# Kernel tuning notes

Hardware: AMD Instinct MI355X
Metric: run time of the kernel (lower is better)

The kernel has to match this reference:

```python
import jax, jax.numpy as jnp
import numpy as np

B, N, D, H = 8, 1024, 768, 12
HD = D // H


def setup_inputs() -> dict:
    key = jax.random.key(0)
    ks = jax.random.split(key, 13)
    s = 0.02
    return {
        "q": jax.random.normal(ks[0], (B, N, D), jnp.float32),
        "k": jax.random.normal(ks[1], (B, N, D), jnp.float32),
        "v": jax.random.normal(ks[2], (B, N, D), jnp.float32),
        "attn_bias": jax.random.normal(ks[3], (B, H, N, N), jnp.float32),
        "attn_mask": jnp.ones((B, N, N), jnp.int32),
        "Wq": jax.random.normal(ks[4], (D, D), jnp.float32) * s,
        "bq": jnp.zeros((D,), jnp.float32),
        "Wk": jax.random.normal(ks[5], (D, D), jnp.float32) * s,
        "bk": jnp.zeros((D,), jnp.float32),
        "Wv": jax.random.normal(ks[6], (D, D), jnp.float32) * s,
        "bv": jnp.zeros((D,), jnp.float32),
        "Wo": jax.random.normal(ks[7], (D, D), jnp.float32) * s,
        "bo": jnp.zeros((D,), jnp.float32),
    }


def reference(q, k, v, attn_bias, attn_mask, Wq, bq, Wk, bk, Wv, bv, Wo, bo):
    scale = jnp.sqrt(jnp.float32(HD))
    # projections; nn.Linear computes x @ W.T + b
    qh = (q @ Wq.T + bq).reshape(B, N, H, HD).transpose(0, 2, 1, 3)  # [B,H,N,hd]
    kh = (k @ Wk.T + bk).reshape(B, N, H, HD).transpose(0, 2, 1, 3)
    vh = (v @ Wv.T + bv).reshape(B, N, H, HD).transpose(0, 2, 1, 3)
    attn = jnp.einsum("bhqd,bhkd->bhqk", qh, kh) / scale
    attn = attn + attn_bias  # Graphormer edge/spatial bias
    attn = jnp.where(attn_mask[:, None, :, :] == 0, -jnp.inf, attn)
    attn = jax.nn.softmax(attn, axis=-1)
    out = jnp.einsum("bhqk,bhkd->bhqd", attn, vh)  # [B,H,N,hd]
    out = out.transpose(0, 2, 1, 3).reshape(B, N, D)
    return out @ Wo.T + bo
```

## Files before the change

### kernel.cpp

```cpp
#include <hip/hip_runtime.h>
#include <hip/hip_bf16.h>

using f32x4  = __attribute__((ext_vector_type(4))) float;
using i32x4  = __attribute__((ext_vector_type(4))) int;
using bf16x8 = __attribute__((ext_vector_type(8))) short;
using bf16x4 = __attribute__((ext_vector_type(4))) short;

constexpr int BATCH = 8, SEQ = 1024, DIM = 768, NHEAD = 12, HDIM = 64;
constexpr int MROWS = BATCH * SEQ;

__device__ __forceinline__ short f2bf(float f) {
    union { float f; unsigned u; } x; x.f = f;
    unsigned r = (x.u + 0x7fffu + ((x.u >> 16) & 1u)) >> 16;
    return (short)r;
}
__device__ __forceinline__ float fexp2(float x) { return __builtin_amdgcn_exp2f(x); }

__device__ __forceinline__ bf16x8 cvt8(const float* p) {
    const f32x4 x0 = *(const f32x4*)p;
    const f32x4 x1 = *(const f32x4*)(p + 4);
    bf16x8 r;
    #pragma unroll
    for (int j = 0; j < 4; ++j) { r[j] = f2bf(x0[j]); r[4 + j] = f2bf(x1[j]); }
    return r;
}

__device__ __forceinline__ long kfrag_addr(int tok, int dd) {
    return ((long)(tok >> 6)) * 4096 + ((tok & 63) >> 4) * 1024 + (dd >> 5) * 512
         + ((dd >> 3) & 3) * 128 + (tok & 15) * 8 + (dd & 7);
}
__device__ __forceinline__ long vfrag_addr(int tok, int dd) {
    return ((long)(tok >> 6)) * 4096 + (dd >> 4) * 1024 + ((tok >> 5) & 1) * 512
         + ((tok >> 3) & 3) * 128 + (dd & 15) * 8 + (tok & 7);
}

__global__ __launch_bounds__(256)
void cvt3(const float* __restrict__ a, const float* __restrict__ b,
          const float* __restrict__ c, short* __restrict__ oa,
          short* __restrict__ ob, short* __restrict__ oc, int n8) {
    const int stride = gridDim.x * 256;
    for (int i = blockIdx.x * 256 + threadIdx.x; i < n8; i += stride) {
        const long base = (long)i * 8;
        *(bf16x8*)(oa + base) = cvt8(a + base);
        *(bf16x8*)(ob + base) = cvt8(b + base);
        *(bf16x8*)(oc + base) = cvt8(c + base);
    }
}

__global__ __launch_bounds__(256)
void cvt4(const float* __restrict__ a, const float* __restrict__ b,
          const float* __restrict__ c, const float* __restrict__ d,
          short* __restrict__ oa, short* __restrict__ ob,
          short* __restrict__ oc, short* __restrict__ od, int n8) {
    const int stride = gridDim.x * 256;
    for (int i = blockIdx.x * 256 + threadIdx.x; i < n8; i += stride) {
        const long base = (long)i * 8;
        *(bf16x8*)(oa + base) = cvt8(a + base);
        *(bf16x8*)(ob + base) = cvt8(b + base);
        *(bf16x8*)(oc + base) = cvt8(c + base);
        *(bf16x8*)(od + base) = cvt8(d + base);
    }
}

__global__ __launch_bounds__(256, 4)
void gemm_qkv(const short* __restrict__ qb, const short* __restrict__ kb,
              const short* __restrict__ vbp,
              const short* __restrict__ Wqb, const short* __restrict__ Wkb,
              const short* __restrict__ Wvb,
              const float* __restrict__ bq, const float* __restrict__ bk,
              const float* __restrict__ bv,
              short* __restrict__ Qp, short* __restrict__ Kp, short* __restrict__ Vp) {
    constexpr int K  = DIM;
    constexpr int NT = DIM / 128;
    __shared__ short As[128][72];
    __shared__ short Bs[128][72];

    const int sub = blockIdx.x % 3;
    const int bid = blockIdx.x / 3;
    const short* A = sub == 0 ? qb : sub == 1 ? kb : vbp;
    const short* W = sub == 0 ? Wqb : sub == 1 ? Wkb : Wvb;
    const float* bias = sub == 0 ? bq : sub == 1 ? bk : bv;

    const int bm = bid / NT, bn = bid % NT;
    const int m0 = bm * 128, n0 = bn * 128;
    const int t = threadIdx.x;
    const int lane = t & 63, w = t >> 6;
    const int wm = (w >> 1) * 64, wn = (w & 1) * 64;
    const int l16 = lane & 15, lg = lane >> 4;

    const int sr = t >> 1, sc = (t & 1) * 16;
    const short* aptr = A + (long)(m0 + sr) * K + sc;
    const short* wptr = W + (long)(n0 + sr) * K + sc;

    bf16x8 ra0 = *(const bf16x8*)(aptr);
    bf16x8 ra1 = *(const bf16x8*)(aptr + 8);
    bf16x8 rw0 = *(const bf16x8*)(wptr);
    bf16x8 rw1 = *(const bf16x8*)(wptr + 8);

    f32x4 acc[4][4] = {};

    for (int k0 = 0; k0 < K; k0 += 32) {
        *(bf16x8*)&As[sr][sc]     = ra0;
        *(bf16x8*)&As[sr][sc + 8] = ra1;
        *(bf16x8*)&Bs[sr][sc]     = rw0;
        *(bf16x8*)&Bs[sr][sc + 8] = rw1;
        if (k0 + 32 < K) {
            ra0 = *(const bf16x8*)(aptr + k0 + 32);
            ra1 = *(const bf16x8*)(aptr + k0 + 40);
            rw0 = *(const bf16x8*)(wptr + k0 + 32);
            rw1 = *(const bf16x8*)(wptr + k0 + 40);
        }
        __syncthreads();

        bf16x8 af[4], bfg[4];
        const int kc = lg * 8;
        #pragma unroll
        for (int mi = 0; mi < 4; ++mi)
            af[mi] = *(const bf16x8*)&As[wm + mi * 16 + l16][kc];
        #pragma unroll
        for (int ni = 0; ni < 4; ++ni)
            bfg[ni] = *(const bf16x8*)&Bs[wn + ni * 16 + l16][kc];
        #pragma unroll
        for (int mi = 0; mi < 4; ++mi)
            #pragma unroll
            for (int ni = 0; ni < 4; ++ni)
                acc[mi][ni] = __builtin_amdgcn_mfma_f32_16x16x32_bf16(
                    af[mi], bfg[ni], acc[mi][ni], 0, 0, 0);
        __syncthreads();
    }

    #pragma unroll
    for (int mi = 0; mi < 4; ++mi) {
        const int row = m0 + wm + mi * 16 + lg * 4;
        const int bb = row / SEQ;
        #pragma unroll
        for (int ni = 0; ni < 4; ++ni) {
            const int col = n0 + wn + ni * 16 + l16;
            const float bv = bias[col];
            const int hh = col >> 6, dd = col & 63;
            #pragma unroll
            for (int j = 0; j < 4; ++j) {
                float val = acc[mi][ni][j] + bv;
                if (sub == 0) {
                    Qp[(long)(row + j) * DIM + col] = f2bf(val * 0.125f);
                } else {
                    const int tok = (row % SEQ) + j;
                    const long pbase = (long)(bb * NHEAD + hh) * 65536;
                    if (sub == 1)
                        Kp[pbase + kfrag_addr(tok, dd)] = f2bf(val);
                    else
                        Vp[pbase + vfrag_addr(tok, dd)] = f2bf(val);
                }
            }
        }
    }
}

__global__ __launch_bounds__(256, 4)
void gemm_out(const short* __restrict__ A, const short* __restrict__ W,
              const float* __restrict__ bias, float* __restrict__ Cout) {
    constexpr int K  = DIM;
    constexpr int NT = DIM / 128;
    __shared__ short As[128][72];
    __shared__ short Bs[128][72];

    const int bm = blockIdx.x / NT, bn = blockIdx.x % NT;
    const int m0 = bm * 128, n0 = bn * 128;
    const int t = threadIdx.x;
    const int lane = t & 63, w = t >> 6;
    const int wm = (w >> 1) * 64, wn = (w & 1) * 64;
    const int l16 = lane & 15, lg = lane >> 4;

    const int sr = t >> 1, sc = (t & 1) * 16;
    const short* aptr = A + (long)(m0 + sr) * K + sc;
    const short* wptr = W + (long)(n0 + sr) * K + sc;

    bf16x8 ra0 = *(const bf16x8*)(aptr);
    bf16x8 ra1 = *(const bf16x8*)(aptr + 8);
    bf16x8 rw0 = *(const bf16x8*)(wptr);
    bf16x8 rw1 = *(const bf16x8*)(wptr + 8);

    f32x4 acc[4][4] = {};

    for (int k0 = 0; k0 < K; k0 += 32) {
        *(bf16x8*)&As[sr][sc]     = ra0;
        *(bf16x8*)&As[sr][sc + 8] = ra1;
        *(bf16x8*)&Bs[sr][sc]     = rw0;
        *(bf16x8*)&Bs[sr][sc + 8] = rw1;
        if (k0 + 32 < K) {
            ra0 = *(const bf16x8*)(aptr + k0 + 32);
            ra1 = *(const bf16x8*)(aptr + k0 + 40);
            rw0 = *(const bf16x8*)(wptr + k0 + 32);
            rw1 = *(const bf16x8*)(wptr + k0 + 40);
        }
        __syncthreads();

        bf16x8 af[4], bfg[4];
        const int kc = lg * 8;
        #pragma unroll
        for (int mi = 0; mi < 4; ++mi)
            af[mi] = *(const bf16x8*)&As[wm + mi * 16 + l16][kc];
        #pragma unroll
        for (int ni = 0; ni < 4; ++ni)
            bfg[ni] = *(const bf16x8*)&Bs[wn + ni * 16 + l16][kc];
        #pragma unroll
        for (int mi = 0; mi < 4; ++mi)
            #pragma unroll
            for (int ni = 0; ni < 4; ++ni)
                acc[mi][ni] = __builtin_amdgcn_mfma_f32_16x16x32_bf16(
                    af[mi], bfg[ni], acc[mi][ni], 0, 0, 0);
        __syncthreads();
    }

    #pragma unroll
    for (int mi = 0; mi < 4; ++mi) {
        const int row = m0 + wm + mi * 16 + lg * 4;
        #pragma unroll
        for (int ni = 0; ni < 4; ++ni) {
            const int col = n0 + wn + ni * 16 + l16;
            const float bv = bias[col];
            #pragma unroll
            for (int j = 0; j < 4; ++j)
                Cout[(long)(row + j) * DIM + col] = acc[mi][ni][j] + bv;
        }
    }
}

__global__ __launch_bounds__(256, 4)
void attn_kernel(const short* __restrict__ Qp, const short* __restrict__ Kt,
                 const short* __restrict__ Vt, const float* __restrict__ bias,
                 const int* __restrict__ mask, short* __restrict__ Op) {
    __shared__ float Bsm[64][68];

    const int d = blockIdx.x;
    const int lgc = (d & 7) * 192 + (d >> 3);
    const int qt = lgc & 15, pair = lgc >> 4;
    const int h = pair % NHEAD, b = pair / NHEAD;

    const int t = threadIdx.x, lane = t & 63, w = t >> 6;
    const int l16 = lane & 15, lg = lane >> 4;
    const int ql = w * 16 + l16;

    const int qrow = qt * 64 + ql;
    const short* qptr = Qp + (long)(b * SEQ + qrow) * DIM + h * HDIM + lg * 8;
    const bf16x8 qf0 = *(const bf16x8*)qptr;
    const bf16x8 qf1 = *(const bf16x8*)(qptr + 32);

    const short* ktile = Kt + (long)pair * 65536 + lane * 8;
    const short* vtile = Vt + (long)pair * 65536 + lane * 8;

    const int srow = t >> 4, scol = (t & 15) * 4;
    const float* bst = bias + ((long)pair * SEQ + qt * 64 + srow) * SEQ + scol;
    const int*   mst = mask + ((long)b * SEQ + qt * 64 + srow) * SEQ + scol;

    short* prow = (short*)&Bsm[ql][0];

    f32x4 acc_o[4] = {};
    float m_run = -1e30f, l_run = 0.f;
    constexpr float L2E = 1.4426950408889634f;

    f32x4 br[4]; i32x4 mr[4];

    auto issue_bm = [&](int kt) {
        #pragma unroll
        for (int i = 0; i < 4; ++i) {
            br[i] = __builtin_nontemporal_load((const f32x4*)(bst + (long)i * 16 * SEQ + kt * 64));
            mr[i] = *(const i32x4*)(mst + (long)i * 16 * SEQ + kt * 64);
        }
    };
    auto write_bm = [&]() {
        #pragma unroll
        for (int i = 0; i < 4; ++i) {
            f32x4 o;
            #pragma unroll
            for (int j = 0; j < 4; ++j) o[j] = mr[i][j] ? br[i][j] : -1e30f;
            *(f32x4*)&Bsm[i * 16 + srow][scol] = o;
        }
    };

    auto compute = [&](int kt) {
        const short* kf = ktile + kt * 4096;
        const short* vf = vtile + kt * 4096;

        f32x4 s[4];
        __builtin_amdgcn_s_setprio(1);
        #pragma unroll
        for (int c = 0; c < 4; ++c) {
            const bf16x8 kb = *(const bf16x8*)(kf + c * 1024);
            f32x4 ci = *(const f32x4*)&Bsm[ql][c * 16 + lg * 4];
            s[c] = __builtin_amdgcn_mfma_f32_16x16x32_bf16(kb, qf0, ci, 0, 0, 0);
        }
        #pragma unroll
        for (int c = 0; c < 4; ++c) {
            const bf16x8 kb = *(const bf16x8*)(kf + c * 1024 + 512);
            s[c] = __builtin_amdgcn_mfma_f32_16x16x32_bf16(kb, qf1, s[c], 0, 0, 0);
        }
        __builtin_amdgcn_s_setprio(0);

        float mt = -1e30f;
        #pragma unroll
        for (int c = 0; c < 4; ++c)
            #pragma unroll
            for (int j = 0; j < 4; ++j)
                mt = fmaxf(mt, s[c][j]);
        mt = fmaxf(mt, __shfl_xor(mt, 16));
        mt = fmaxf(mt, __shfl_xor(mt, 32));
        const float mn = fmaxf(m_run, mt);
        const float alpha = fexp2((m_run - mn) * L2E);
        m_run = mn;
        const float nm = -mn * L2E;

        float lt = 0.f;
        #pragma unroll
        for (int c = 0; c < 4; ++c) {
            bf16x4 pk;
            #pragma unroll
            for (int j = 0; j < 4; ++j) {
                const float e = fexp2(fmaf(s[c][j], L2E, nm));
                lt += e;
                pk[j] = f2bf(e);
            }
            *(bf16x4*)(prow + c * 16 + lg * 4) = pk;
        }
        lt += __shfl_xor(lt, 16);
        lt += __shfl_xor(lt, 32);
        l_run = l_run * alpha + lt;

        float al[4];
        #pragma unroll
        for (int j = 0; j < 4; ++j) al[j] = __shfl(alpha, lg * 4 + j);
        #pragma unroll
        for (int df = 0; df < 4; ++df)
            #pragma unroll
            for (int j = 0; j < 4; ++j)
                acc_o[df][j] *= al[j];

        const bf16x8 pa0 = *(const bf16x8*)(prow + lg * 8);
        const bf16x8 pa1 = *(const bf16x8*)(prow + 32 + lg * 8);
        __builtin_amdgcn_s_setprio(1);
        #pragma unroll
        for (int df = 0; df < 4; ++df) {
            const bf16x8 vb = *(const bf16x8*)(vf + df * 1024);
            acc_o[df] = __builtin_amdgcn_mfma_f32_16x16x32_bf16(pa0, vb, acc_o[df], 0, 0, 0);
        }
        #pragma unroll
        for (int df = 0; df < 4; ++df) {
            const bf16x8 vb = *(const bf16x8*)(vf + df * 1024 + 512);
            acc_o[df] = __builtin_amdgcn_mfma_f32_16x16x32_bf16(pa1, vb, acc_o[df], 0, 0, 0);
        }
        __builtin_amdgcn_s_setprio(0);
    };

    issue_bm(0);
    write_bm();
    __syncthreads();

    for (int kt = 0; kt < 16; ++kt) {
        if (kt < 15) issue_bm(kt + 1);
        compute(kt);
        if (kt < 15) {
            __syncthreads();
            write_bm();
            __syncthreads();
        }
    }

    float linv[4];
    #pragma unroll
    for (int j = 0; j < 4; ++j)
        linv[j] = 1.f / fmaxf(__shfl(l_run, lg * 4 + j), 1e-20f);

    #pragma unroll
    for (int df = 0; df < 4; ++df) {
        #pragma unroll
        for (int j = 0; j < 4; ++j) {
            const float val = acc_o[df][j] * linv[j];
            const int row = b * SEQ + qt * 64 + w * 16 + lg * 4 + j;
            const int col = h * HDIM + df * 16 + l16;
            Op[(long)row * DIM + col] = f2bf(val);
        }
    }
}

extern "C" void kernel_launch(void* const* d_in, const int* in_sizes, int n_in,
                              void* d_out, int out_size, void* d_ws, size_t ws_size,
                              hipStream_t stream) {
    const float* q         = (const float*)d_in[0];
    const float* k         = (const float*)d_in[1];
    const float* v         = (const float*)d_in[2];
    const float* attn_bias = (const float*)d_in[3];
    const int*   attn_mask = (const int*)d_in[4];
    const float* Wq = (const float*)d_in[5];
    const float* bq = (const float*)d_in[6];
    const float* Wk = (const float*)d_in[7];
    const float* bk = (const float*)d_in[8];
    const float* Wv = (const float*)d_in[9];
    const float* bv = (const float*)d_in[10];
    const float* Wo = (const float*)d_in[11];
    const float* bo = (const float*)d_in[12];
    float* out = (float*)d_out;

    const long NED = (long)MROWS * DIM;
    const long WED = (long)DIM * DIM;
    short* Qp  = (short*)d_ws;
    short* Kp  = Qp + NED;
    short* Vp  = Kp + NED;
    short* Op  = Vp + NED;
    short* qb  = Op + NED;
    short* kb  = qb + NED;
    short* vb  = kb + NED;
    short* Wqb = vb + NED;
    short* Wkb = Wqb + WED;
    short* Wvb = Wkb + WED;
    short* Wob = Wvb + WED;

    const dim3 blk(256);

    cvt3<<<2048, blk, 0, stream>>>(q, k, v, qb, kb, vb, (int)(NED / 8));
    cvt4<<<288, blk, 0, stream>>>(Wq, Wk, Wv, Wo, Wqb, Wkb, Wvb, Wob, (int)(WED / 8));

    const int gemm_grid = (MROWS / 128) * (DIM / 128);
    gemm_qkv<<<3 * gemm_grid, blk, 0, stream>>>(qb, kb, vb, Wqb, Wkb, Wvb,
                                                bq, bk, bv, Qp, Kp, Vp);

    const int attn_grid = BATCH * NHEAD * (SEQ / 64);
    attn_kernel<<<attn_grid, blk, 0, stream>>>(Qp, Kp, Vp, attn_bias, attn_mask, Op);

    gemm_out<<<gemm_grid, blk, 0, stream>>>(Op, Wob, bo, out);
}
```

Baseline: 273.8 us.

## Double-buffer attention bias tile in LDS and merge conversion kernels

The attention kernel now keeps two LDS buffers for the masked bias/probability tile, so the next tile is written to the other buffer while the current one is in use. This removes one of the two barriers per key tile, and the bias prefetch is issued one iteration earlier. The two fp32-to-bf16 conversion kernels are merged into one launch to save launch overhead. In exchange, LDS use per block doubles (about 35KB), which may reduce occupancy, and register pressure rises because of the earlier prefetch.

```diff
diff --git a/kernel.cpp b/kernel.cpp
--- a/kernel.cpp
+++ b/kernel.cpp
@@ -35,30 +35,27 @@
 }
 
 __global__ __launch_bounds__(256)
-void cvt3(const float* __restrict__ a, const float* __restrict__ b,
-          const float* __restrict__ c, short* __restrict__ oa,
-          short* __restrict__ ob, short* __restrict__ oc, int n8) {
+void cvt_all(const float* __restrict__ q, const float* __restrict__ k,
+             const float* __restrict__ v,
+             const float* __restrict__ Wq, const float* __restrict__ Wk,
+             const float* __restrict__ Wv, const float* __restrict__ Wo,
+             short* __restrict__ qb, short* __restrict__ kb, short* __restrict__ vb,
+             short* __restrict__ Wqb, short* __restrict__ Wkb,
+             short* __restrict__ Wvb, short* __restrict__ Wob,
+             int nbig8, int nsml8) {
     const int stride = gridDim.x * 256;
-    for (int i = blockIdx.x * 256 + threadIdx.x; i < n8; i += stride) {
+    for (int i = blockIdx.x * 256 + threadIdx.x; i < nbig8; i += stride) {
         const long base = (long)i * 8;
-        *(bf16x8*)(oa + base) = cvt8(a + base);
-        *(bf16x8*)(ob + base) = cvt8(b + base);
-        *(bf16x8*)(oc + base) = cvt8(c + base);
-    }
-}
-
-__global__ __launch_bounds__(256)
-void cvt4(const float* __restrict__ a, const float* __restrict__ b,
-          const float* __restrict__ c, const float* __restrict__ d,
-          short* __restrict__ oa, short* __restrict__ ob,
-          short* __restrict__ oc, short* __restrict__ od, int n8) {
-    const int stride = gridDim.x * 256;
-    for (int i = blockIdx.x * 256 + threadIdx.x; i < n8; i += stride) {
+        *(bf16x8*)(qb + base) = cvt8(q + base);
+        *(bf16x8*)(kb + base) = cvt8(k + base);
+        *(bf16x8*)(vb + base) = cvt8(v + base);
+    }
+    for (int i = blockIdx.x * 256 + threadIdx.x; i < nsml8; i += stride) {
         const long base = (long)i * 8;
-        *(bf16x8*)(oa + base) = cvt8(a + base);
-        *(bf16x8*)(ob + base) = cvt8(b + base);
-        *(bf16x8*)(oc + base) = cvt8(c + base);
-        *(bf16x8*)(od + base) = cvt8(d + base);
+        *(bf16x8*)(Wqb + base) = cvt8(Wq + base);
+        *(bf16x8*)(Wkb + base) = cvt8(Wk + base);
+        *(bf16x8*)(Wvb + base) = cvt8(Wv + base);
+        *(bf16x8*)(Wob + base) = cvt8(Wo + base);
     }
 }
 
@@ -230,7 +227,7 @@
 void attn_kernel(const short* __restrict__ Qp, const short* __restrict__ Kt,
                  const short* __restrict__ Vt, const float* __restrict__ bias,
                  const int* __restrict__ mask, short* __restrict__ Op) {
-    __shared__ float Bsm[64][68];
+    __shared__ float Bsm[2][64][68];
 
     const int d = blockIdx.x;
     const int lgc = (d & 7) * 192 + (d >> 3);
@@ -253,8 +250,6 @@
     const float* bst = bias + ((long)pair * SEQ + qt * 64 + srow) * SEQ + scol;
     const int*   mst = mask + ((long)b * SEQ + qt * 64 + srow) * SEQ + scol;
 
-    short* prow = (short*)&Bsm[ql][0];
-
     f32x4 acc_o[4] = {};
     float m_run = -1e30f, l_run = 0.f;
     constexpr float L2E = 1.4426950408889634f;
@@ -268,26 +263,27 @@
             mr[i] = *(const i32x4*)(mst + (long)i * 16 * SEQ + kt * 64);
         }
     };
-    auto write_bm = [&]() {
+    auto write_bm = [&](int buf) {
         #pragma unroll
         for (int i = 0; i < 4; ++i) {
             f32x4 o;
             #pragma unroll
             for (int j = 0; j < 4; ++j) o[j] = mr[i][j] ? br[i][j] : -1e30f;
-            *(f32x4*)&Bsm[i * 16 + srow][scol] = o;
+            *(f32x4*)&Bsm[buf][i * 16 + srow][scol] = o;
         }
     };
 
-    auto compute = [&](int kt) {
+    auto compute = [&](int kt, int buf) {
         const short* kf = ktile + kt * 4096;
         const short* vf = vtile + kt * 4096;
+        short* prow = (short*)&Bsm[buf][ql][0];
 
         f32x4 s[4];
         __builtin_amdgcn_s_setprio(1);
         #pragma unroll
         for (int c = 0; c < 4; ++c) {
             const bf16x8 kb = *(const bf16x8*)(kf + c * 1024);
-            f32x4 ci = *(const f32x4*)&Bsm[ql][c * 16 + lg * 4];
+            f32x4 ci = *(const f32x4*)&Bsm[buf][ql][c * 16 + lg * 4];
             s[c] = __builtin_amdgcn_mfma_f32_16x16x32_bf16(kb, qf0, ci, 0, 0, 0);
         }
         #pragma unroll
@@ -352,16 +348,18 @@
     };
 
     issue_bm(0);
-    write_bm();
+    write_bm(0);
+    issue_bm(1);
     __syncthreads();
 
+    int cur = 0;
     for (int kt = 0; kt < 16; ++kt) {
-        if (kt < 15) issue_bm(kt + 1);
-        compute(kt);
+        compute(kt, cur);
         if (kt < 15) {
+            write_bm(cur ^ 1);
+            if (kt < 14) issue_bm(kt + 2);
             __syncthreads();
-            write_bm();
-            __syncthreads();
+            cur ^= 1;
         }
     }
 
@@ -416,8 +414,9 @@
 
     const dim3 blk(256);
 
-    cvt3<<<2048, blk, 0, stream>>>(q, k, v, qb, kb, vb, (int)(NED / 8));
-    cvt4<<<288, blk, 0, stream>>>(Wq, Wk, Wv, Wo, Wqb, Wkb, Wvb, Wob, (int)(WED / 8));
+    cvt_all<<<2048, blk, 0, stream>>>(q, k, v, Wq, Wk, Wv, Wo,
+                                      qb, kb, vb, Wqb, Wkb, Wvb, Wob,
+                                      (int)(NED / 8), (int)(WED / 8));
 
     const int gemm_grid = (MROWS / 128) * (DIM / 128);
     gemm_qkv<<<3 * gemm_grid, blk, 0, stream>>>(qb, kb, vb, Wqb, Wkb, Wvb,
```

New measurement: 260.1 us. -5.0%, faster.
